# Kernel tuning notes

Hardware: AMD Instinct MI355X
Metric: run time of the kernel (lower is better)

## Reference

```python
import jax, jax.numpy as jnp
import numpy as np

B, N, D, K = 1024, 36, 256, 8  # batch, num_features(fixed 36 by docstring), embed_size, text_K


def setup_inputs() -> dict:
    key = jax.random.key(0)
    ks = jax.random.split(key, 5)
    texts = jax.random.normal(ks[0], (B, N, D), dtype=jnp.float32)
    # Xavier-uniform-style init matching module.init_weights()
    r_k = np.sqrt(6.0) / np.sqrt(D + D)
    r_v = np.sqrt(6.0) / np.sqrt(D + K)
    r_u = np.sqrt(6.0) / np.sqrt(K + 1)
    W = jax.random.uniform(ks[1], (K, D, D), minval=-r_k, maxval=r_k, dtype=jnp.float32)
    Wb = jnp.zeros((K, D), dtype=jnp.float32)
    V1w = jax.random.uniform(ks[2], (K, D), minval=-r_v, maxval=r_v, dtype=jnp.float32)
    V1b = jnp.zeros((K,), dtype=jnp.float32)
    V2w = jax.random.uniform(ks[3], (K, D), minval=-r_v, maxval=r_v, dtype=jnp.float32)
    V2b = jnp.zeros((K,), dtype=jnp.float32)
    Uw = jax.random.uniform(ks[4], (K,), minval=-r_u, maxval=r_u, dtype=jnp.float32)
    Ub = jnp.zeros((), dtype=jnp.float32)
    return {"texts": texts, "W": W, "Wb": Wb, "V1w": V1w, "V1b": V1b,
            "V2w": V2w, "V2b": V2b, "Uw": Uw, "Ub": Ub}


def reference(texts, W, Wb, V1w, V1b, V2w, V2b, Uw, Ub):
    # bilinear term: (W_k x_n + b_k) . x_m  -> [B,K,N,N]
    Wx = jnp.einsum('kcd,bnd->bknc', W, texts) + Wb[None, :, None, :]
    first = jnp.einsum('bknc,bmc->bknm', Wx, texts)
    # outer-sum term: V1.x_n + V2.x_m (per k)
    v1 = jnp.einsum('kd,bnd->bkn', V1w, texts) + V1b[None, :, None]  # [B,K,N]
    v2 = jnp.einsum('kd,bmd->bkm', V2w, texts) + V2b[None, :, None]  # [B,K,N]
    T = jnp.tanh(first + v1[..., None] + v2[:, :, None, :])  # [B,K,N,N]
    # faithful to torch: flatten [K,N,N] contiguously then view as (N*N, K)
    flat = T.reshape(T.shape[0], N * N, K)
    logits = (flat @ Uw + Ub).reshape(T.shape[0], N, N)
    return jax.nn.softmax(logits, axis=-1)
```

## Files before the change

### kernel.cpp

```cpp
#include <hip/hip_runtime.h>
#include <math.h>

#define NB 1024
#define NF 36
#define ED 256
#define NK 8
#define NN2 1296
#define QPK 162

typedef _Float16 f16;
typedef f16 f16x8 __attribute__((ext_vector_type(8)));
typedef float f32x4 __attribute__((ext_vector_type(4)));

#define WXSTR 136
#define WXHSZ 13056
#define NFRAG 1536

#define XH_OFF  0
#define WXH_OFF 24576
#define V_OFF   (24576 + WXHSZ)
#define SMEM_MAIN (V_OFF + (72 + 72 + 9 + 324) * 4)

#define PVH_OFF 0
#define PVL_OFF 8192
#define PP_OFF  16384
#define SMEM_PREP 28672

#define TWO_LOG2E 2.8853900817779268f
#define C1F (0.0625f * TWO_LOG2E)

__device__ __forceinline__ f32x4 mfma16(f16x8 a, f16x8 b, f32x4 c) {
    return __builtin_amdgcn_mfma_f32_16x16x32_f16(a, b, c, 0, 0, 0);
}

__global__ __launch_bounds__(256, 4) void prep_all(
    const float* __restrict__ W, f16x8* __restrict__ WfH,
    const float* __restrict__ texts, f16x8* __restrict__ XfH, f16x8* __restrict__ XfL,
    const float* __restrict__ V1w, const float* __restrict__ V1b,
    const float* __restrict__ V2w, const float* __restrict__ V2b,
    const float* __restrict__ Wb, float* __restrict__ v12)
{
    extern __shared__ char psmem[];
    const int blk = blockIdx.x;
    const int t = threadIdx.x;
    const int wave = t >> 6, lane = t & 63;

    if (blk < 128) {
        const int k = blk >> 4, ct = blk & 15;
        f16* Wl = (f16*)psmem;
        {
            const int r = t >> 4, seg = t & 15;
            const float* src = W + ((size_t)(k * 256 + ct * 16 + r)) * 256 + seg * 16;
            f16* d = Wl + r * 264 + seg * 16;
            #pragma unroll
            for (int j4 = 0; j4 < 4; ++j4) {
                float4 a = ((const float4*)src)[j4];
                d[j4 * 4 + 0] = (f16)(a.x * 16.0f);
                d[j4 * 4 + 1] = (f16)(a.y * 16.0f);
                d[j4 * 4 + 2] = (f16)(a.z * 16.0f);
                d[j4 * 4 + 3] = (f16)(a.w * 16.0f);
            }
        }
        __syncthreads();
        f16x8* dst = WfH + (size_t)(k * 16 + ct) * 8 * 64;
        #pragma unroll
        for (int e0 = 0; e0 < 2; ++e0) {
            const int e = t + e0 * 256;
            const int kc = e >> 6, el = e & 63, qd = el >> 4, l15 = el & 15;
            dst[e] = *(const f16x8*)(Wl + l15 * 264 + (kc * 4 + qd) * 8);
        }
        return;
    }

    f16x8* VfH = (f16x8*)(psmem + PVH_OFF);
    f16x8* VfL = (f16x8*)(psmem + PVL_OFF);
    f32x4* Pp  = (f32x4*)(psmem + PP_OFF);

    const int b = blk - 128;
    const float* xb = texts + (size_t)b * NF * ED;

    #pragma unroll
    for (int i0 = 0; i0 < 2; ++i0) {
        int i = t + i0 * 256;
        int kc = (i >> 6) & 7, ln = i & 63;
        int q = ln >> 4, col = ln & 15;
        int which = col >> 3, kk = col & 7;
        const float* src  = (which ? V2w : V1w) + kk * 256 + kc * 32 + q * 8;
        const float* srcb = Wb + kk * 256 + kc * 32 + q * 8;
        f16x8 hi, lo;
        #pragma unroll
        for (int j = 0; j < 8; ++j) {
            float sv = src[j] + (which ? srcb[j] : 0.f);
            sv *= 16.0f;
            f16 h = (f16)sv;
            hi[j] = h;
            lo[j] = (f16)(sv - (float)h);
        }
        VfH[i] = hi;
        VfL[i] = lo;
    }

    f16x8 FH[6], FL[6];
    #pragma unroll
    for (int i0 = 0; i0 < 6; ++i0) {
        int i = t + i0 * 256;
        int rt = i >> 9, kc = (i >> 6) & 7;
        int q = lane >> 4, l15 = lane & 15;
        int row = rt * 16 + l15;
        f16x8 hi, lo;
        if (row < NF) {
            const float* s = xb + row * ED + kc * 32 + q * 8;
            float4 a = *(const float4*)s;
            float4 c = *(const float4*)(s + 4);
            float v[8] = {a.x, a.y, a.z, a.w, c.x, c.y, c.z, c.w};
            #pragma unroll
            for (int j = 0; j < 8; ++j) {
                f16 h = (f16)v[j];
                hi[j] = h;
                lo[j] = (f16)(v[j] - (float)h);
            }
        } else {
            #pragma unroll
            for (int j = 0; j < 8; ++j) { hi[j] = (f16)0.f; lo[j] = (f16)0.f; }
        }
        FH[i0] = hi;
        FL[i0] = lo;
        XfH[(size_t)b * NFRAG + i] = hi;
        XfL[(size_t)b * NFRAG + i] = lo;
    }
    __syncthreads();

    f32x4 pacc[3];
    #pragma unroll
    for (int rt = 0; rt < 3; ++rt) pacc[rt] = (f32x4){0.f, 0.f, 0.f, 0.f};
    #pragma unroll
    for (int rt = 0; rt < 3; ++rt) {
        #pragma unroll
        for (int s = 0; s < 2; ++s) {
            const int i0 = rt * 2 + s;
            const int kc = wave + 4 * s;
            f16x8 bh = VfH[kc * 64 + lane];
            f16x8 bl = VfL[kc * 64 + lane];
            pacc[rt] = mfma16(FH[i0], bh, pacc[rt]);
            pacc[rt] = mfma16(FH[i0], bl, pacc[rt]);
            pacc[rt] = mfma16(FL[i0], bh, pacc[rt]);
        }
    }
    #pragma unroll
    for (int rt = 0; rt < 3; ++rt)
        Pp[(wave * 3 + rt) * 64 + lane] = pacc[rt];
    __syncthreads();

    if (wave < 3) {
        f32x4 acc = Pp[(0 * 3 + wave) * 64 + lane];
        #pragma unroll
        for (int w = 1; w < 4; ++w) acc += Pp[(w * 3 + wave) * 64 + lane];
        const int q = lane >> 4, l15 = lane & 15;
        const int which = l15 >> 3, kk = l15 & 7;
        const float bias = which ? V2b[kk] : V1b[kk];
        #pragma unroll
        for (int r = 0; r < 4; ++r) {
            const int n = wave * 16 + q * 4 + r;
            if (n < NF)
                v12[((size_t)b * 16 + l15) * NF + n] = acc[r] * 0.0625f + bias;
        }
    }
}

__global__ __launch_bounds__(256, 4) void ntn_main(
    const f16x8* __restrict__ XfHG, const f16x8* __restrict__ XfLG,
    const f16x8* __restrict__ WfH,
    const float* __restrict__ v12,
    const float* __restrict__ Uw, const float* __restrict__ Ubp,
    float* __restrict__ out)
{
    extern __shared__ char smem[];
    f16x8* Xh   = (f16x8*)(smem + XH_OFF);
    f16*   Wxh  = (f16*)(smem + WXH_OFF);
    float* v1s2 = (float*)(smem + V_OFF);
    float* v2s2 = v1s2 + 72;
    float* Uws  = v1s2 + 144;
    float* Ls   = v1s2 + 153;

    const int id  = blockIdx.x;
    const int xcd = id & 7;
    const int rem = id >> 3;
    const int kp  = rem & 3;
    const int b   = ((rem >> 2) << 3) | xcd;
    const int k0  = kp * 2;

    const int t    = threadIdx.x;
    const int wave = t >> 6;
    const int lane = t & 63;
    const int quad = lane >> 4;
    const int l15  = lane & 15;

    const f16x8* Xlg = XfLG + (size_t)b * NFRAG;

    {
        const f16x8* gh = XfHG + (size_t)b * NFRAG;
        #pragma unroll
        for (int i = 0; i < 6; ++i) Xh[t + i * 256] = gh[t + i * 256];
    }
    if (t < 144) {
        const int r = t / 36, n = t - r * 36;
        const int which = r & 1, kq = r >> 1;
        float v = v12[((size_t)b * 16 + which * 8 + (k0 + kq)) * NF + n] * TWO_LOG2E;
        (which ? v2s2 : v1s2)[kq * 36 + n] = v;
    }
    if (t < 8) Uws[t] = Uw[t];
    if (t == 8) Uws[8] = Ubp[0];
    __syncthreads();

    const f16x8* Wk0 = WfH + (size_t)k0 * 8192;
    const f16x8* Wk1 = Wk0 + 8192;

    f32x4 sacc[2][3];
    #pragma unroll
    for (int kk = 0; kk < 2; ++kk)
        #pragma unroll
        for (int it = 0; it < 3; ++it) sacc[kk][it] = (f32x4){0.f, 0.f, 0.f, 0.f};

    for (int h = 0; h < 2; ++h) {
        f32x4 acc[3][2][2];
        #pragma unroll
        for (int i = 0; i < 3; ++i)
            #pragma unroll
            for (int j = 0; j < 2; ++j) {
                acc[i][j][0] = (f32x4){0.f, 0.f, 0.f, 0.f};
                acc[i][j][1] = (f32x4){0.f, 0.f, 0.f, 0.f};
            }
        const int ct0 = h * 8 + wave;
        const int ct1 = ct0 + 4;
        #pragma unroll 2
        for (int kc = 0; kc < 8; ++kc) {
            f16x8 w00 = Wk0[(ct0 * 8 + kc) * 64 + lane];
            f16x8 w01 = Wk0[(ct1 * 8 + kc) * 64 + lane];
            f16x8 w10 = Wk1[(ct0 * 8 + kc) * 64 + lane];
            f16x8 w11 = Wk1[(ct1 * 8 + kc) * 64 + lane];
            #pragma unroll
            for (int rt = 0; rt < 3; ++rt) {
                f16x8 ah = Xh[(rt * 8 + kc) * 64 + lane];
                acc[rt][0][0] = mfma16(ah, w00, acc[rt][0][0]);
                acc[rt][1][0] = mfma16(ah, w01, acc[rt][1][0]);
                acc[rt][0][1] = mfma16(ah, w10, acc[rt][0][1]);
                acc[rt][1][1] = mfma16(ah, w11, acc[rt][1][1]);
            }
        }
        #pragma unroll
        for (int kk = 0; kk < 2; ++kk) {
            __syncthreads();
            #pragma unroll
            for (int rt = 0; rt < 3; ++rt)
                #pragma unroll
                for (int j2 = 0; j2 < 2; ++j2) {
                    const int cl = (j2 ? (wave + 4) : wave) * 16 + l15;
                    #pragma unroll
                    for (int r = 0; r < 4; ++r) {
                        const int row = rt * 16 + quad * 4 + r;
                        Wxh[row * WXSTR + cl] = (f16)(acc[rt][j2][kk][r]);
                    }
                }
            __syncthreads();
            #pragma unroll
            for (int it = 0; it < 3; ++it) {
                const int p = wave + it * 4;
                if (p < 9) {
                    const int nt = p / 3, mt = p % 3;
                    const f16* wxh_p = Wxh + (nt * 16 + l15) * WXSTR + quad * 8;
                    #pragma unroll
                    for (int kc2 = 0; kc2 < 4; ++kc2) {
                        f16x8 pah = *(const f16x8*)(wxh_p + kc2 * 32);
                        f16x8 pbh = Xh[(mt * 8 + h * 4 + kc2) * 64 + lane];
                        f16x8 pbl = Xlg[(mt * 8 + h * 4 + kc2) * 64 + lane];
                        sacc[kk][it] = mfma16(pah, pbh, sacc[kk][it]);
                        sacc[kk][it] = mfma16(pah, pbl, sacc[kk][it]);
                    }
                }
            }
        }
    }

    __syncthreads();
    float* Ts = (float*)Wxh;
    #pragma unroll
    for (int kk = 0; kk < 2; ++kk)
        #pragma unroll
        for (int it = 0; it < 3; ++it) {
            const int p = wave + it * 4;
            if (p < 9) {
                const int nt = p / 3, mt = p % 3;
                const int m = mt * 16 + l15;
                if (m < NF) {
                    #pragma unroll
                    for (int r = 0; r < 4; ++r) {
                        const int n = nt * 16 + quad * 4 + r;
                        if (n < NF) {
                            float x = sacc[kk][it][r] * C1F
                                      + v1s2[kk * 36 + n] + v2s2[kk * 36 + m];
                            float e = exp2f(x);
                            const int idx = kk * NN2 + n * NF + m;
                            Ts[idx + (idx >> 3)] = 1.f - 2.f / (e + 1.f);
                        }
                    }
                }
            }
        }
    __syncthreads();
    #pragma unroll
    for (int u0 = 0; u0 < 2; ++u0) {
        const int u = t + u0 * 256;
        if (u < 324) {
            const float* tp = Ts + u * 9;
            float lg = Uws[8];
            #pragma unroll
            for (int j = 0; j < 8; ++j) lg += Uws[j] * tp[j];
            Ls[u] = lg;
        }
    }
    __syncthreads();
    #pragma unroll
    for (int rr0 = 0; rr0 < 3; ++rr0) {
        const int rr = wave + rr0 * 4;
        if (rr < 9) {
            float v = (lane < NF) ? Ls[rr * 36 + lane] : -INFINITY;
            float mx = v;
            #pragma unroll
            for (int off = 32; off > 0; off >>= 1) mx = fmaxf(mx, __shfl_xor(mx, off));
            float e = (lane < NF) ? __expf(v - mx) : 0.f;
            float sm = e;
            #pragma unroll
            for (int off = 32; off > 0; off >>= 1) sm += __shfl_xor(sm, off);
            if (lane < NF)
                out[(size_t)b * NN2 + kp * 324 + rr * 36 + lane] = e / sm;
        }
    }
}

extern "C" void kernel_launch(void* const* d_in, const int* in_sizes, int n_in,
                              void* d_out, int out_size, void* d_ws, size_t ws_size,
                              hipStream_t stream) {
    const float* texts = (const float*)d_in[0];
    const float* W     = (const float*)d_in[1];
    const float* Wb    = (const float*)d_in[2];
    const float* V1w   = (const float*)d_in[3];
    const float* V1b   = (const float*)d_in[4];
    const float* V2w   = (const float*)d_in[5];
    const float* V2b   = (const float*)d_in[6];
    const float* Uw    = (const float*)d_in[7];
    const float* Ub    = (const float*)d_in[8];

    char* ws = (char*)d_ws;
    f16x8* WfH = (f16x8*)ws;
    f16x8* XfH = (f16x8*)(ws + (1 << 20));
    f16x8* XfL = (f16x8*)(ws + (1 << 20) + (size_t)NB * NFRAG * 16);
    float* v12 = (float*)(ws + (1 << 20) + (size_t)2 * NB * NFRAG * 16);
    float* outp = (float*)d_out;

    hipFuncSetAttribute((const void*)prep_all,
                        hipFuncAttributeMaxDynamicSharedMemorySize, SMEM_PREP);
    hipFuncSetAttribute((const void*)ntn_main,
                        hipFuncAttributeMaxDynamicSharedMemorySize, SMEM_MAIN);

    prep_all<<<128 + NB, 256, SMEM_PREP, stream>>>(W, WfH, texts, XfH, XfL,
                                                   V1w, V1b, V2w, V2b, Wb, v12);
    ntn_main<<<NB * NK / 2, 256, SMEM_MAIN, stream>>>(XfH, XfL, WfH, v12, Uw, Ub, outp);
}
```

Measured before the change: 203.5 us.

## Double-buffer Wx tile and overlap second-half GEMM with first-half bilinear MFMAs

```diff
diff --git a/kernel.cpp b/kernel.cpp
--- a/kernel.cpp
+++ b/kernel.cpp
@@ -14,11 +14,12 @@
 
 #define WXSTR 136
 #define WXHSZ 13056
+#define WXF   6528
 #define NFRAG 1536
 
 #define XH_OFF  0
 #define WXH_OFF 24576
-#define V_OFF   (24576 + WXHSZ)
+#define V_OFF   (24576 + 2 * WXHSZ)
 #define SMEM_MAIN (V_OFF + (72 + 72 + 9 + 324) * 4)
 
 #define PVH_OFF 0
@@ -167,7 +168,24 @@
     }
 }
 
-__global__ __launch_bounds__(256, 4) void ntn_main(
+#define P2_TILE(IT, H) do {                                                   \
+    const int p_ = wave + (IT) * 4;                                           \
+    if (p_ < 18) {                                                            \
+        const int kkp_ = p_ / 9, q9_ = p_ - kkp_ * 9;                         \
+        const int nt_ = q9_ / 3, mt_ = q9_ - nt_ * 3;                         \
+        const f16* wp_ = Wxh + kkp_ * WXF + (nt_ * 16 + l15) * WXSTR + quad * 8; \
+        _Pragma("unroll")                                                     \
+        for (int kc2 = 0; kc2 < 4; ++kc2) {                                   \
+            f16x8 pah = *(const f16x8*)(wp_ + kc2 * 32);                      \
+            f16x8 pbh = Xh[(mt_ * 8 + (H) * 4 + kc2) * 64 + lane];            \
+            f16x8 pbl = Xlg[(mt_ * 8 + (H) * 4 + kc2) * 64 + lane];           \
+            sacc[IT] = mfma16(pah, pbh, sacc[IT]);                            \
+            sacc[IT] = mfma16(pah, pbl, sacc[IT]);                            \
+        }                                                                     \
+    }                                                                         \
+} while (0)
+
+__global__ __launch_bounds__(256, 3) void ntn_main(
     const f16x8* __restrict__ XfHG, const f16x8* __restrict__ XfLG,
     const f16x8* __restrict__ WfH,
     const float* __restrict__ v12,
@@ -215,23 +233,21 @@
     const f16x8* Wk0 = WfH + (size_t)k0 * 8192;
     const f16x8* Wk1 = Wk0 + 8192;
 
-    f32x4 sacc[2][3];
-    #pragma unroll
-    for (int kk = 0; kk < 2; ++kk)
-        #pragma unroll
-        for (int it = 0; it < 3; ++it) sacc[kk][it] = (f32x4){0.f, 0.f, 0.f, 0.f};
-
-    for (int h = 0; h < 2; ++h) {
-        f32x4 acc[3][2][2];
-        #pragma unroll
-        for (int i = 0; i < 3; ++i)
-            #pragma unroll
-            for (int j = 0; j < 2; ++j) {
-                acc[i][j][0] = (f32x4){0.f, 0.f, 0.f, 0.f};
-                acc[i][j][1] = (f32x4){0.f, 0.f, 0.f, 0.f};
-            }
-        const int ct0 = h * 8 + wave;
-        const int ct1 = ct0 + 4;
+    f32x4 sacc[5];
+    #pragma unroll
+    for (int it = 0; it < 5; ++it) sacc[it] = (f32x4){0.f, 0.f, 0.f, 0.f};
+
+    f32x4 acc[3][2][2];
+
+    #pragma unroll
+    for (int i = 0; i < 3; ++i)
+        #pragma unroll
+        for (int j = 0; j < 2; ++j) {
+            acc[i][j][0] = (f32x4){0.f, 0.f, 0.f, 0.f};
+            acc[i][j][1] = (f32x4){0.f, 0.f, 0.f, 0.f};
+        }
+    {
+        const int ct0 = wave, ct1 = wave + 4;
         #pragma unroll 2
         for (int kc = 0; kc < 8; ++kc) {
             f16x8 w00 = Wk0[(ct0 * 8 + kc) * 64 + lane];
@@ -247,65 +263,95 @@
                 acc[rt][1][1] = mfma16(ah, w11, acc[rt][1][1]);
             }
         }
-        #pragma unroll
-        for (int kk = 0; kk < 2; ++kk) {
-            __syncthreads();
-            #pragma unroll
-            for (int rt = 0; rt < 3; ++rt)
+    }
+    #pragma unroll
+    for (int kk = 0; kk < 2; ++kk)
+        #pragma unroll
+        for (int rt = 0; rt < 3; ++rt)
+            #pragma unroll
+            for (int j2 = 0; j2 < 2; ++j2) {
+                const int cl = (j2 ? (wave + 4) : wave) * 16 + l15;
                 #pragma unroll
-                for (int j2 = 0; j2 < 2; ++j2) {
-                    const int cl = (j2 ? (wave + 4) : wave) * 16 + l15;
-                    #pragma unroll
-                    for (int r = 0; r < 4; ++r) {
-                        const int row = rt * 16 + quad * 4 + r;
-                        Wxh[row * WXSTR + cl] = (f16)(acc[rt][j2][kk][r]);
+                for (int r = 0; r < 4; ++r) {
+                    const int row = rt * 16 + quad * 4 + r;
+                    Wxh[kk * WXF + row * WXSTR + cl] = (f16)(acc[rt][j2][kk][r]);
+                }
+            }
+    __syncthreads();
+
+    #pragma unroll
+    for (int i = 0; i < 3; ++i)
+        #pragma unroll
+        for (int j = 0; j < 2; ++j) {
+            acc[i][j][0] = (f32x4){0.f, 0.f, 0.f, 0.f};
+            acc[i][j][1] = (f32x4){0.f, 0.f, 0.f, 0.f};
+        }
+    {
+        const int ct0 = 8 + wave, ct1 = 12 + wave;
+        #pragma unroll
+        for (int step = 0; step < 8; ++step) {
+            f16x8 w00 = Wk0[(ct0 * 8 + step) * 64 + lane];
+            f16x8 w01 = Wk0[(ct1 * 8 + step) * 64 + lane];
+            f16x8 w10 = Wk1[(ct0 * 8 + step) * 64 + lane];
+            f16x8 w11 = Wk1[(ct1 * 8 + step) * 64 + lane];
+            #pragma unroll
+            for (int rt = 0; rt < 3; ++rt) {
+                f16x8 ah = Xh[(rt * 8 + step) * 64 + lane];
+                acc[rt][0][0] = mfma16(ah, w00, acc[rt][0][0]);
+                acc[rt][1][0] = mfma16(ah, w01, acc[rt][1][0]);
+                acc[rt][0][1] = mfma16(ah, w10, acc[rt][0][1]);
+                acc[rt][1][1] = mfma16(ah, w11, acc[rt][1][1]);
+            }
+            if (step < 5) P2_TILE(step, 0);
+        }
+    }
+    __syncthreads();
+
+    #pragma unroll
+    for (int kk = 0; kk < 2; ++kk)
+        #pragma unroll
+        for (int rt = 0; rt < 3; ++rt)
+            #pragma unroll
+            for (int j2 = 0; j2 < 2; ++j2) {
+                const int cl = (j2 ? (wave + 4) : wave) * 16 + l15;
+                #pragma unroll
+                for (int r = 0; r < 4; ++r) {
+                    const int row = rt * 16 + quad * 4 + r;
+                    Wxh[kk * WXF + row * WXSTR + cl] = (f16)(acc[rt][j2][kk][r]);
+                }
+            }
+    __syncthreads();
+
+    P2_TILE(0, 1);
+    P2_TILE(1, 1);
+    P2_TILE(2, 1);
+    P2_TILE(3, 1);
+    P2_TILE(4, 1);
+    __syncthreads();
+
+    float* Ts = (float*)Wxh;
+    #pragma unroll
+    for (int it = 0; it < 5; ++it) {
+        const int p = wave + it * 4;
+        if (p < 18) {
+            const int kkp = p / 9, q9 = p - kkp * 9;
+            const int nt = q9 / 3, mt = q9 - nt * 3;
+            const int m = mt * 16 + l15;
+            if (m < NF) {
+                #pragma unroll
+                for (int r = 0; r < 4; ++r) {
+                    const int n = nt * 16 + quad * 4 + r;
+                    if (n < NF) {
+                        float x = sacc[it][r] * C1F
+                                  + v1s2[kkp * 36 + n] + v2s2[kkp * 36 + m];
+                        float e = exp2f(x);
+                        const int idx = kkp * NN2 + n * NF + m;
+                        Ts[idx + (idx >> 3)] = 1.f - 2.f / (e + 1.f);
                     }
                 }
-            __syncthreads();
-            #pragma unroll
-            for (int it = 0; it < 3; ++it) {
-                const int p = wave + it * 4;
-                if (p < 9) {
-                    const int nt = p / 3, mt = p % 3;
-                    const f16* wxh_p = Wxh + (nt * 16 + l15) * WXSTR + quad * 8;
-                    #pragma unroll
-                    for (int kc2 = 0; kc2 < 4; ++kc2) {
-                        f16x8 pah = *(const f16x8*)(wxh_p + kc2 * 32);
-                        f16x8 pbh = Xh[(mt * 8 + h * 4 + kc2) * 64 + lane];
-                        f16x8 pbl = Xlg[(mt * 8 + h * 4 + kc2) * 64 + lane];
-                        sacc[kk][it] = mfma16(pah, pbh, sacc[kk][it]);
-                        sacc[kk][it] = mfma16(pah, pbl, sacc[kk][it]);
-                    }
-                }
-            }
-        }
-    }
-
-    __syncthreads();
-    float* Ts = (float*)Wxh;
-    #pragma unroll
-    for (int kk = 0; kk < 2; ++kk)
-        #pragma unroll
-        for (int it = 0; it < 3; ++it) {
-            const int p = wave + it * 4;
-            if (p < 9) {
-                const int nt = p / 3, mt = p % 3;
-                const int m = mt * 16 + l15;
-                if (m < NF) {
-                    #pragma unroll
-                    for (int r = 0; r < 4; ++r) {
-                        const int n = nt * 16 + quad * 4 + r;
-                        if (n < NF) {
-                            float x = sacc[kk][it][r] * C1F
-                                      + v1s2[kk * 36 + n] + v2s2[kk * 36 + m];
-                            float e = exp2f(x);
-                            const int idx = kk * NN2 + n * NF + m;
-                            Ts[idx + (idx >> 3)] = 1.f - 2.f / (e + 1.f);
-                        }
-                    }
-                }
-            }
-        }
+            }
+        }
+    }
     __syncthreads();
     #pragma unroll
     for (int u0 = 0; u0 < 2; ++u0) {
```

Result: slower. 213.1 us (+4.7%).
